# Optimization experiments

Measured on AMD Instinct MI355X. Metric: run time of the kernel, lower is better.

The kernel has to match this reference:

```python
import jax, jax.numpy as jnp
import numpy as np

B, V, J, H, W = 32, 2, 17, 128, 128
TEMP = 0.05   # SoftArgmax2D softmax_temp
EPS = 1e-12


def _soft_argmax(hm):
    # hm: (B*V, J, H, W) -> homogeneous coords (B*V, 3, J), per-joint max value
    bv, j, h, w = hm.shape
    p = jax.nn.softmax(hm.reshape(bv, j, h * w) / TEMP, axis=-1).reshape(bv, j, h, w)
    xs = jnp.arange(w, dtype=hm.dtype)
    ys = jnp.arange(h, dtype=hm.dtype)
    x = jnp.einsum('bjhw,w->bj', p, xs)
    y = jnp.einsum('bjhw,h->bj', p, ys)
    coords = jnp.stack([x, y, jnp.ones_like(x)], axis=1)  # (bv, 3, j)
    maxv = hm.max(axis=(-2, -1))
    return coords, maxv


def _skew(t):
    # t: (..., 3) -> skew-symmetric (..., 3, 3), matches -t_mat^T + t_mat in source
    tx, ty, tz = t[..., 0], t[..., 1], t[..., 2]
    z = jnp.zeros_like(tx)
    return jnp.stack([jnp.stack([z, -tz, ty], -1),
                      jnp.stack([tz, z, -tx], -1),
                      jnp.stack([-ty, tx, z], -1)], -2)


def _forward(origin_hms, AP_K, AP_T, LAT_K, LAT_T):
    K = jnp.stack([AP_K, LAT_K], axis=1)              # (B,V,3,3)
    T = jnp.stack([AP_T, LAT_T], axis=1)              # (B,V,4,4)
    R = T[:, :, :3, :3]
    t_std = T[:, :, :3, 3]                            # (B,V,3) standard_cam_T

    # fundamental matrices for all ordered pairs: cam1 = view j, cam2 = view i
    r = jnp.einsum('bimk,bjnk->bijmn', R, R)          # R_i @ R_j^T
    t = t_std[:, :, None, :] - jnp.einsum('bijmn,bjn->bijm', r, t_std)
    M = jnp.einsum('bijmn,bijnk->bijmk', _skew(t), r)
    invK = jnp.linalg.inv(K)
    # F = invK_i^T @ [t]x @ r @ invK_j
    F = jnp.einsum('bipm,bijpq,bjql->bijml', invK, M, invK)  # (B,V,V,3,3)

    coords, maxv = _soft_argmax(origin_hms)           # (B*V,3,J), (B*V,J)
    inv_aff = jnp.diag(jnp.asarray([4.0, 4.0, 1.0], dtype=origin_hms.dtype))  # inverse of 0.25 scale
    img = jnp.einsum('mn,bvnj->bvmj', inv_aff, coords.reshape(B, V, 3, J))
    confi = maxv.reshape(B, V, J)

    # epipolar distances, fully vectorized over (b, i, j) pairs
    l = jnp.einsum('bijmn,bjnk->bijmk', F, img)       # epipolar lines in view i from joints of view j
    cv = img[:, :, None]                              # (B,V,1,3,J)
    num = jnp.sum(cv * l, axis=3) ** 2                # (B,V,V,J)
    lp = jnp.einsum('bijnm,bink->bijmk', F, img)      # F^T @ cv_joints
    div = l[..., 0, :] ** 2 + l[..., 1, :] ** 2 + lp[..., 0, :] ** 2 + lp[..., 1, :] ** 2
    dist_full = jnp.sqrt(num / (div + EPS))           # (B,V,V,J)

    others = np.asarray([[j for j in range(V) if j != i] for i in range(V)])  # (V,V-1)
    ii = np.repeat(np.arange(V)[:, None], V - 1, axis=1)
    distances = dist_full[:, ii, others]              # (B,V,V-1,J)

    # stand-in for ViewWeightNet: confidence minus mean epipolar error, softmax over views
    score = confi - distances.mean(axis=2)            # (B,V,J)
    vw = jax.nn.softmax(score, axis=1)                # (B,V,J)

    mv = jnp.where(maxv > 0.01, maxv, 1e6).reshape(B * V, J, 1, 1)
    hms_norm = origin_hms / mv
    hm4 = hms_norm.reshape(B, V, J, H, W)

    # cat order: self heatmap first, then other views (matches get_warp_weight / cat_hm layout)
    order = np.asarray([[i] + [j for j in range(V) if j != i] for i in range(V)])  # (V,V)
    cat_hm = hm4[:, order]                            # (B,V,V,J,H,W); identity-warp stand-in for CamFusionModule
    ww = vw[:, order]                                 # (B,V,V,J) warp weights
    fused_hm = jnp.sum(ww[..., None, None] * cat_hm, axis=2).reshape(B * V, J, H, W)

    coords2, _ = _soft_argmax(fused_hm)
    img2 = jnp.einsum('mn,bvnj->bvmj', inv_aff, coords2.reshape(B, V, 3, J))
    return img2[:, :, :2, :], fused_hm


def setup_inputs() -> dict:
    key = jax.random.key(0)
    k1, k2, k3, k4, k5 = jax.random.split(key, 5)
    hms = jax.random.uniform(k1, (B * V, J, H, W), dtype=jnp.float32)

    def make_K(k):
        f = 1000.0 + jax.random.normal(k, (B,)) * 10.0
        Km = jnp.zeros((B, 3, 3), dtype=jnp.float32)
        Km = Km.at[:, 0, 0].set(f).at[:, 1, 1].set(f)
        Km = Km.at[:, 0, 2].set(256.0).at[:, 1, 2].set(256.0).at[:, 2, 2].set(1.0)
        return Km

    def make_T(k):
        A = jax.random.normal(k, (B, 3, 3))
        Q, _ = jnp.linalg.qr(A)
        Q = Q * jnp.linalg.det(Q)[:, None, None]  # force det = +1 (proper rotation)
        t = jax.random.normal(jax.random.fold_in(k, 1), (B, 3, 1)) * 0.1 + jnp.asarray([0.0, 0.0, 5.0]).reshape(3, 1)
        bottom = jnp.tile(jnp.asarray([[[0.0, 0.0, 0.0, 1.0]]]), (B, 1, 1))
        return jnp.concatenate([jnp.concatenate([Q, t], axis=2), bottom], axis=1).astype(jnp.float32)

    return {"origin_hms": hms, "AP_K": make_K(k2), "AP_T": make_T(k3),
            "LAT_K": make_K(k4), "LAT_T": make_T(k5)}


def reference(origin_hms, AP_K, AP_T, LAT_K, LAT_T):
    return _forward(origin_hms, AP_K, AP_T, LAT_K, LAT_T)
```

## Files before the change

kernel.cpp:

```cpp
#include <hip/hip_runtime.h>
#include <math.h>

#define NB 32
#define NV 2
#define NJ 17
#define NH 128
#define NW 128
#define MAPN (NH * NW)
#define MAPN4 (MAPN / 4)
#define NMAPS (NB * NV * NJ)
#define NBJ (NB * NJ)
#define OUT0N (NB * NV * 2 * NJ)
#define INV_TEMP 20.0f
#define EPS_D 1e-12f

typedef float vfloat4 __attribute__((ext_vector_type(4)));

__device__ __forceinline__ float waveMax(float v) {
#pragma unroll
    for (int off = 32; off > 0; off >>= 1)
        v = fmaxf(v, __shfl_xor(v, off, 64));
    return v;
}
__device__ __forceinline__ float waveSum(float v) {
#pragma unroll
    for (int off = 32; off > 0; off >>= 1)
        v += __shfl_xor(v, off, 64);
    return v;
}

__device__ __forceinline__ void inv3(const float K[3][3], float o[3][3]) {
    const float a = K[0][0], b = K[0][1], c = K[0][2];
    const float d = K[1][0], e = K[1][1], f = K[1][2];
    const float g = K[2][0], h = K[2][1], i = K[2][2];
    const float A =  (e * i - f * h);
    const float Bv = -(d * i - f * g);
    const float C =  (d * h - e * g);
    const float det = a * A + b * Bv + c * C;
    const float id = 1.0f / det;
    o[0][0] = A * id;  o[0][1] = -(b * i - c * h) * id;  o[0][2] = (b * f - c * e) * id;
    o[1][0] = Bv * id; o[1][1] = (a * i - c * g) * id;   o[1][2] = -(a * f - c * d) * id;
    o[2][0] = C * id;  o[2][1] = -(a * h - b * g) * id;  o[2][2] = (a * e - b * d) * id;
}

__global__ __launch_bounds__(512, 2) void k_one(const float* __restrict__ hms,
                                                const float* __restrict__ APK,
                                                const float* __restrict__ APT,
                                                const float* __restrict__ LATK,
                                                const float* __restrict__ LATT,
                                                float* __restrict__ out) {
    const int blk = blockIdx.x;
    const int b = blk / NJ, j = blk % NJ;
    const int tid = threadIdx.x;
    const int wid = tid >> 6, lane = tid & 63;

    float F[2][3][3];
    {
        float Km[2][3][3], R[2][3][3], tr[2][3], iK[2][3][3];
        for (int r = 0; r < 3; ++r)
            for (int c = 0; c < 3; ++c) {
                Km[0][r][c] = APK[b * 9 + r * 3 + c];
                Km[1][r][c] = LATK[b * 9 + r * 3 + c];
                R[0][r][c] = APT[b * 16 + r * 4 + c];
                R[1][r][c] = LATT[b * 16 + r * 4 + c];
            }
        for (int r = 0; r < 3; ++r) {
            tr[0][r] = APT[b * 16 + r * 4 + 3];
            tr[1][r] = LATT[b * 16 + r * 4 + 3];
        }
        inv3(Km[0], iK[0]);
        inv3(Km[1], iK[1]);

        for (int i = 0; i < 2; ++i) {
            const int jj = 1 - i;
            float r[3][3];
            for (int m = 0; m < 3; ++m)
                for (int n = 0; n < 3; ++n)
                    r[m][n] = R[i][m][0] * R[jj][n][0] + R[i][m][1] * R[jj][n][1] + R[i][m][2] * R[jj][n][2];
            float tv[3];
            for (int m = 0; m < 3; ++m)
                tv[m] = tr[i][m] - (r[m][0] * tr[jj][0] + r[m][1] * tr[jj][1] + r[m][2] * tr[jj][2]);
            const float S[3][3] = {{0.f, -tv[2], tv[1]}, {tv[2], 0.f, -tv[0]}, {-tv[1], tv[0], 0.f}};
            float M[3][3];
            for (int m = 0; m < 3; ++m)
                for (int n = 0; n < 3; ++n)
                    M[m][n] = S[m][0] * r[0][n] + S[m][1] * r[1][n] + S[m][2] * r[2][n];
            float tmp[3][3];
            for (int p = 0; p < 3; ++p)
                for (int l = 0; l < 3; ++l)
                    tmp[p][l] = M[p][0] * iK[jj][0][l] + M[p][1] * iK[jj][1][l] + M[p][2] * iK[jj][2][l];
            for (int m = 0; m < 3; ++m)
                for (int l = 0; l < 3; ++l)
                    F[i][m][l] = iK[i][0][m] * tmp[0][l] + iK[i][1][m] * tmp[1][l] + iK[i][2][m] * tmp[2][l];
        }
    }

    const int idx0 = (b * 2 + 0) * NJ + j;
    const int idx1 = (b * 2 + 1) * NJ + j;
    const size_t m0 = (size_t)idx0 * MAPN4;
    const size_t m1 = (size_t)idx1 * MAPN4;
    const float4* A  = (const float4*)hms + m0;
    const float4* Bp = (const float4*)hms + m1;

    float4 va[8];
    float mx0 = -1e30f, s0 = 0.f, sx0 = 0.f, sy0 = 0.f;
    float mx1 = -1e30f, s1 = 0.f, sx1 = 0.f, sy1 = 0.f;
#pragma unroll
    for (int u = 0; u < 8; ++u) {
        const int i4 = tid + u * 512;
        const float4 v = A[i4];
        const float4 w = Bp[i4];
        va[u] = v;
        const int e0 = i4 * 4;
        const float hh = (float)(e0 >> 7);
        const float ww = (float)(e0 & 127);
        {
            mx0 = fmaxf(mx0, fmaxf(fmaxf(v.x, v.y), fmaxf(v.z, v.w)));
            const float ea = __expf((v.x - 1.0f) * INV_TEMP);
            const float eb = __expf((v.y - 1.0f) * INV_TEMP);
            const float ec = __expf((v.z - 1.0f) * INV_TEMP);
            const float ed = __expf((v.w - 1.0f) * INV_TEMP);
            const float se = (ea + eb) + (ec + ed);
            s0 += se; sy0 += se * hh;
            sx0 += ea * ww + eb * (ww + 1.f) + ec * (ww + 2.f) + ed * (ww + 3.f);
        }
        {
            mx1 = fmaxf(mx1, fmaxf(fmaxf(w.x, w.y), fmaxf(w.z, w.w)));
            const float ea = __expf((w.x - 1.0f) * INV_TEMP);
            const float eb = __expf((w.y - 1.0f) * INV_TEMP);
            const float ec = __expf((w.z - 1.0f) * INV_TEMP);
            const float ed = __expf((w.w - 1.0f) * INV_TEMP);
            const float se = (ea + eb) + (ec + ed);
            s1 += se; sy1 += se * hh;
            sx1 += ea * ww + eb * (ww + 1.f) + ec * (ww + 2.f) + ed * (ww + 3.f);
        }
    }

    __shared__ float red[8][8];
    mx0 = waveMax(mx0); mx1 = waveMax(mx1);
    s0 = waveSum(s0); sx0 = waveSum(sx0); sy0 = waveSum(sy0);
    s1 = waveSum(s1); sx1 = waveSum(sx1); sy1 = waveSum(sy1);
    if (lane == 0) {
        red[0][wid] = mx0; red[1][wid] = s0; red[2][wid] = sx0; red[3][wid] = sy0;
        red[4][wid] = mx1; red[5][wid] = s1; red[6][wid] = sx1; red[7][wid] = sy1;
    }
    __syncthreads();
    float M0 = red[0][0], S0 = red[1][0], SX0 = red[2][0], SY0 = red[3][0];
    float M1 = red[4][0], S1 = red[5][0], SX1 = red[6][0], SY1 = red[7][0];
#pragma unroll
    for (int w = 1; w < 8; ++w) {
        M0 = fmaxf(M0, red[0][w]); S0 += red[1][w]; SX0 += red[2][w]; SY0 += red[3][w];
        M1 = fmaxf(M1, red[4][w]); S1 += red[5][w]; SX1 += red[6][w]; SY1 += red[7][w];
    }

    float w0, w1;
    {
        const float conf[2] = {M0, M1};
        float img[2][3];
        img[0][0] = 4.0f * (SX0 / S0); img[0][1] = 4.0f * (SY0 / S0); img[0][2] = 1.0f;
        img[1][0] = 4.0f * (SX1 / S1); img[1][1] = 4.0f * (SY1 / S1); img[1][2] = 1.0f;

        float score[2];
        for (int i = 0; i < 2; ++i) {
            const int jj = 1 - i;
            const float l0 = F[i][0][0] * img[jj][0] + F[i][0][1] * img[jj][1] + F[i][0][2] * img[jj][2];
            const float l1 = F[i][1][0] * img[jj][0] + F[i][1][1] * img[jj][1] + F[i][1][2] * img[jj][2];
            const float l2 = F[i][2][0] * img[jj][0] + F[i][2][1] * img[jj][1] + F[i][2][2] * img[jj][2];
            const float sdot = img[i][0] * l0 + img[i][1] * l1 + img[i][2] * l2;
            const float num = sdot * sdot;
            const float lp0 = F[i][0][0] * img[i][0] + F[i][1][0] * img[i][1] + F[i][2][0] * img[i][2];
            const float lp1 = F[i][0][1] * img[i][0] + F[i][1][1] * img[i][1] + F[i][2][1] * img[i][2];
            const float dv = l0 * l0 + l1 * l1 + lp0 * lp0 + lp1 * lp1;
            score[i] = conf[i] - sqrtf(num / (dv + EPS_D));
        }
        const float mS = fmaxf(score[0], score[1]);
        const float e0w = __expf(score[0] - mS), e1w = __expf(score[1] - mS);
        const float inv = 1.0f / (e0w + e1w);
        const float mv0 = conf[0] > 0.01f ? conf[0] : 1e6f;
        const float mv1 = conf[1] > 0.01f ? conf[1] : 1e6f;
        w0 = (e0w * inv) / mv0;
        w1 = (e1w * inv) / mv1;
    }

    float* outhm = out + OUT0N;
    vfloat4* O0 = reinterpret_cast<vfloat4*>(outhm) + m0;
    vfloat4* O1 = reinterpret_cast<vfloat4*>(outhm) + m1;

    float s = 0.f, sx = 0.f, sy = 0.f;
#pragma unroll
    for (int u = 0; u < 8; ++u) {
        const int i4 = tid + u * 512;
        const float4 a = va[u];
        const float4 c = Bp[i4];
        vfloat4 f;
        f.x = w0 * a.x + w1 * c.x;
        f.y = w0 * a.y + w1 * c.y;
        f.z = w0 * a.z + w1 * c.z;
        f.w = w0 * a.w + w1 * c.w;
        __builtin_nontemporal_store(f, &O0[i4]);
        __builtin_nontemporal_store(f, &O1[i4]);
        const int e0 = i4 * 4;
        const float hh = (float)(e0 >> 7);
        const float ww = (float)(e0 & 127);
        const float ea = __expf((f.x - 1.0f) * INV_TEMP);
        const float eb = __expf((f.y - 1.0f) * INV_TEMP);
        const float ec = __expf((f.z - 1.0f) * INV_TEMP);
        const float ed = __expf((f.w - 1.0f) * INV_TEMP);
        const float se = (ea + eb) + (ec + ed);
        s += se; sy += se * hh;
        sx += ea * ww + eb * (ww + 1.f) + ec * (ww + 2.f) + ed * (ww + 3.f);
    }

    __syncthreads();
    s = waveSum(s); sx = waveSum(sx); sy = waveSum(sy);
    if (lane == 0) { red[0][wid] = s; red[1][wid] = sx; red[2][wid] = sy; }
    __syncthreads();
    if (tid == 0) {
        float S = red[0][0], SX = red[1][0], SY = red[2][0];
#pragma unroll
        for (int w = 1; w < 8; ++w) { S += red[0][w]; SX += red[1][w]; SY += red[2][w]; }
        const float x4 = 4.0f * (SX / S);
        const float y4 = 4.0f * (SY / S);
        out[((b * 2 + 0) * 2 + 0) * NJ + j] = x4;
        out[((b * 2 + 0) * 2 + 1) * NJ + j] = y4;
        out[((b * 2 + 1) * 2 + 0) * NJ + j] = x4;
        out[((b * 2 + 1) * 2 + 1) * NJ + j] = y4;
    }
}

extern "C" void kernel_launch(void* const* d_in, const int* in_sizes, int n_in,
                              void* d_out, int out_size, void* d_ws, size_t ws_size,
                              hipStream_t stream) {
    const float* hms  = (const float*)d_in[0];
    const float* APK  = (const float*)d_in[1];
    const float* APT  = (const float*)d_in[2];
    const float* LATK = (const float*)d_in[3];
    const float* LATT = (const float*)d_in[4];
    float* out = (float*)d_out;

    k_one<<<NBJ, 512, 0, stream>>>(hms, APK, APT, LATK, LATT, out);
}
```

Before: 136.6 us.

## Split fused kernel into four chunked kernels for more parallelism via workspace

```diff
diff --git a/kernel.cpp b/kernel.cpp
--- a/kernel.cpp
+++ b/kernel.cpp
@@ -14,6 +14,16 @@
 #define INV_TEMP 20.0f
 #define EPS_D 1e-12f
 
+#define S_CHUNKS 4
+#define S_F4 (MAPN4 / S_CHUNKS)
+#define F_CHUNKS 8
+#define F_F4 (MAPN4 / F_CHUNKS)
+
+#define WS_STATS_B (NMAPS * S_CHUNKS * 16)
+#define WS_W_B (NBJ * 2 * 4)
+#define WS_F_B (NBJ * F_CHUNKS * 16)
+#define WS_NEEDED (WS_STATS_B + WS_W_B + WS_F_B)
+
 typedef float vfloat4 __attribute__((ext_vector_type(4)));
 
 __device__ __forceinline__ float waveMax(float v) {
@@ -41,6 +51,210 @@
     o[0][0] = A * id;  o[0][1] = -(b * i - c * h) * id;  o[0][2] = (b * f - c * e) * id;
     o[1][0] = Bv * id; o[1][1] = (a * i - c * g) * id;   o[1][2] = -(a * f - c * d) * id;
     o[2][0] = C * id;  o[2][1] = -(a * h - b * g) * id;  o[2][2] = (a * e - b * d) * id;
+}
+
+__global__ __launch_bounds__(256, 4) void k_stats(const float* __restrict__ hms,
+                                                  float* __restrict__ ws) {
+    const int blk = blockIdx.x;
+    const int mi = blk >> 2, c = blk & 3;
+    const int tid = threadIdx.x, wid = tid >> 6, lane = tid & 63;
+    const float4* A = (const float4*)hms + (size_t)mi * MAPN4 + (size_t)c * S_F4;
+
+    float mx = -1e30f, s = 0.f, sx = 0.f, sy = 0.f;
+#pragma unroll
+    for (int k = 0; k < 4; ++k) {
+        const int i4 = tid + k * 256;
+        const float4 v = A[i4];
+        const int e0 = (c * S_F4 + i4) * 4;
+        const float hh = (float)(e0 >> 7);
+        const float ww = (float)(e0 & 127);
+        mx = fmaxf(mx, fmaxf(fmaxf(v.x, v.y), fmaxf(v.z, v.w)));
+        const float ea = __expf((v.x - 1.0f) * INV_TEMP);
+        const float eb = __expf((v.y - 1.0f) * INV_TEMP);
+        const float ec = __expf((v.z - 1.0f) * INV_TEMP);
+        const float ed = __expf((v.w - 1.0f) * INV_TEMP);
+        const float se = (ea + eb) + (ec + ed);
+        s += se; sy += se * hh;
+        sx += ea * ww + eb * (ww + 1.f) + ec * (ww + 2.f) + ed * (ww + 3.f);
+    }
+
+    mx = waveMax(mx); s = waveSum(s); sx = waveSum(sx); sy = waveSum(sy);
+    __shared__ float red[4][4];
+    if (lane == 0) { red[0][wid] = mx; red[1][wid] = s; red[2][wid] = sx; red[3][wid] = sy; }
+    __syncthreads();
+    if (tid == 0) {
+        float M = red[0][0], S = red[1][0], SX = red[2][0], SY = red[3][0];
+#pragma unroll
+        for (int w = 1; w < 4; ++w) {
+            M = fmaxf(M, red[0][w]); S += red[1][w]; SX += red[2][w]; SY += red[3][w];
+        }
+        ((float4*)ws)[blk] = make_float4(M, S, SX, SY);
+    }
+}
+
+__global__ void k_weights(const float* __restrict__ ws_stats,
+                          const float* __restrict__ APK, const float* __restrict__ APT,
+                          const float* __restrict__ LATK, const float* __restrict__ LATT,
+                          float* __restrict__ wsw) {
+    const int bj = blockIdx.x * 64 + threadIdx.x;
+    if (bj >= NBJ) return;
+    const int b = bj / NJ, j = bj % NJ;
+
+    float conf[2], img[2][3];
+    const float4* st = (const float4*)ws_stats;
+#pragma unroll
+    for (int v = 0; v < 2; ++v) {
+        const int mi = (b * 2 + v) * NJ + j;
+        float M = -1e30f, S = 0.f, SX = 0.f, SY = 0.f;
+#pragma unroll
+        for (int c = 0; c < S_CHUNKS; ++c) {
+            const float4 p = st[mi * S_CHUNKS + c];
+            M = fmaxf(M, p.x); S += p.y; SX += p.z; SY += p.w;
+        }
+        conf[v] = M;
+        img[v][0] = 4.0f * (SX / S);
+        img[v][1] = 4.0f * (SY / S);
+        img[v][2] = 1.0f;
+    }
+
+    float F[2][3][3];
+    {
+        float Km[2][3][3], R[2][3][3], tr[2][3], iK[2][3][3];
+        for (int r = 0; r < 3; ++r)
+            for (int cc = 0; cc < 3; ++cc) {
+                Km[0][r][cc] = APK[b * 9 + r * 3 + cc];
+                Km[1][r][cc] = LATK[b * 9 + r * 3 + cc];
+                R[0][r][cc] = APT[b * 16 + r * 4 + cc];
+                R[1][r][cc] = LATT[b * 16 + r * 4 + cc];
+            }
+        for (int r = 0; r < 3; ++r) {
+            tr[0][r] = APT[b * 16 + r * 4 + 3];
+            tr[1][r] = LATT[b * 16 + r * 4 + 3];
+        }
+        inv3(Km[0], iK[0]);
+        inv3(Km[1], iK[1]);
+
+        for (int i = 0; i < 2; ++i) {
+            const int jj = 1 - i;
+            float r[3][3];
+            for (int m = 0; m < 3; ++m)
+                for (int n = 0; n < 3; ++n)
+                    r[m][n] = R[i][m][0] * R[jj][n][0] + R[i][m][1] * R[jj][n][1] + R[i][m][2] * R[jj][n][2];
+            float tv[3];
+            for (int m = 0; m < 3; ++m)
+                tv[m] = tr[i][m] - (r[m][0] * tr[jj][0] + r[m][1] * tr[jj][1] + r[m][2] * tr[jj][2]);
+            const float S[3][3] = {{0.f, -tv[2], tv[1]}, {tv[2], 0.f, -tv[0]}, {-tv[1], tv[0], 0.f}};
+            float M[3][3];
+            for (int m = 0; m < 3; ++m)
+                for (int n = 0; n < 3; ++n)
+                    M[m][n] = S[m][0] * r[0][n] + S[m][1] * r[1][n] + S[m][2] * r[2][n];
+            float tmp[3][3];
+            for (int p = 0; p < 3; ++p)
+                for (int l = 0; l < 3; ++l)
+                    tmp[p][l] = M[p][0] * iK[jj][0][l] + M[p][1] * iK[jj][1][l] + M[p][2] * iK[jj][2][l];
+            for (int m = 0; m < 3; ++m)
+                for (int l = 0; l < 3; ++l)
+                    F[i][m][l] = iK[i][0][m] * tmp[0][l] + iK[i][1][m] * tmp[1][l] + iK[i][2][m] * tmp[2][l];
+        }
+    }
+
+    float score[2];
+#pragma unroll
+    for (int i = 0; i < 2; ++i) {
+        const int jj = 1 - i;
+        const float l0 = F[i][0][0] * img[jj][0] + F[i][0][1] * img[jj][1] + F[i][0][2] * img[jj][2];
+        const float l1 = F[i][1][0] * img[jj][0] + F[i][1][1] * img[jj][1] + F[i][1][2] * img[jj][2];
+        const float l2 = F[i][2][0] * img[jj][0] + F[i][2][1] * img[jj][1] + F[i][2][2] * img[jj][2];
+        const float sdot = img[i][0] * l0 + img[i][1] * l1 + img[i][2] * l2;
+        const float num = sdot * sdot;
+        const float lp0 = F[i][0][0] * img[i][0] + F[i][1][0] * img[i][1] + F[i][2][0] * img[i][2];
+        const float lp1 = F[i][0][1] * img[i][0] + F[i][1][1] * img[i][1] + F[i][2][1] * img[i][2];
+        const float dv = l0 * l0 + l1 * l1 + lp0 * lp0 + lp1 * lp1;
+        score[i] = conf[i] - sqrtf(num / (dv + EPS_D));
+    }
+    const float mS = fmaxf(score[0], score[1]);
+    const float e0w = __expf(score[0] - mS), e1w = __expf(score[1] - mS);
+    const float inv = 1.0f / (e0w + e1w);
+    const float mv0 = conf[0] > 0.01f ? conf[0] : 1e6f;
+    const float mv1 = conf[1] > 0.01f ? conf[1] : 1e6f;
+    wsw[bj * 2 + 0] = (e0w * inv) / mv0;
+    wsw[bj * 2 + 1] = (e1w * inv) / mv1;
+}
+
+__global__ __launch_bounds__(256, 4) void k_fuse(const float* __restrict__ hms,
+                                                 const float* __restrict__ wsw,
+                                                 float* __restrict__ out,
+                                                 float* __restrict__ wsf) {
+    const int blk = blockIdx.x;
+    const int bj = blk >> 3, c = blk & 7;
+    const int b = bj / NJ, j = bj % NJ;
+    const int tid = threadIdx.x, wid = tid >> 6, lane = tid & 63;
+
+    const float w0 = wsw[bj * 2 + 0];
+    const float w1 = wsw[bj * 2 + 1];
+
+    const size_t m0 = ((size_t)(b * 2 + 0) * NJ + j) * MAPN4;
+    const size_t m1 = ((size_t)(b * 2 + 1) * NJ + j) * MAPN4;
+    const float4* A  = (const float4*)hms + m0 + (size_t)c * F_F4;
+    const float4* Bp = (const float4*)hms + m1 + (size_t)c * F_F4;
+    float* outhm = out + OUT0N;
+    vfloat4* O0 = reinterpret_cast<vfloat4*>(outhm) + m0 + (size_t)c * F_F4;
+    vfloat4* O1 = reinterpret_cast<vfloat4*>(outhm) + m1 + (size_t)c * F_F4;
+
+    float s = 0.f, sx = 0.f, sy = 0.f;
+#pragma unroll
+    for (int k = 0; k < 2; ++k) {
+        const int i4 = tid + k * 256;
+        const float4 a = A[i4];
+        const float4 cc = Bp[i4];
+        vfloat4 f;
+        f.x = w0 * a.x + w1 * cc.x;
+        f.y = w0 * a.y + w1 * cc.y;
+        f.z = w0 * a.z + w1 * cc.z;
+        f.w = w0 * a.w + w1 * cc.w;
+        __builtin_nontemporal_store(f, &O0[i4]);
+        __builtin_nontemporal_store(f, &O1[i4]);
+        const int e0 = (c * F_F4 + i4) * 4;
+        const float hh = (float)(e0 >> 7);
+        const float ww = (float)(e0 & 127);
+        const float ea = __expf((f.x - 1.0f) * INV_TEMP);
+        const float eb = __expf((f.y - 1.0f) * INV_TEMP);
+        const float ec = __expf((f.z - 1.0f) * INV_TEMP);
+        const float ed = __expf((f.w - 1.0f) * INV_TEMP);
+        const float se = (ea + eb) + (ec + ed);
+        s += se; sy += se * hh;
+        sx += ea * ww + eb * (ww + 1.f) + ec * (ww + 2.f) + ed * (ww + 3.f);
+    }
+
+    s = waveSum(s); sx = waveSum(sx); sy = waveSum(sy);
+    __shared__ float red[3][4];
+    if (lane == 0) { red[0][wid] = s; red[1][wid] = sx; red[2][wid] = sy; }
+    __syncthreads();
+    if (tid == 0) {
+        float S = red[0][0], SX = red[1][0], SY = red[2][0];
+#pragma unroll
+        for (int w = 1; w < 4; ++w) { S += red[0][w]; SX += red[1][w]; SY += red[2][w]; }
+        ((float4*)wsf)[blk] = make_float4(S, SX, SY, 0.f);
+    }
+}
+
+__global__ void k_out(const float* __restrict__ wsf, float* __restrict__ out) {
+    const int bj = blockIdx.x * 64 + threadIdx.x;
+    if (bj >= NBJ) return;
+    const int b = bj / NJ, j = bj % NJ;
+    const float4* p = (const float4*)wsf + bj * F_CHUNKS;
+    float S = 0.f, SX = 0.f, SY = 0.f;
+#pragma unroll
+    for (int c = 0; c < F_CHUNKS; ++c) {
+        const float4 q = p[c];
+        S += q.x; SX += q.y; SY += q.z;
+    }
+    const float x4 = 4.0f * (SX / S);
+    const float y4 = 4.0f * (SY / S);
+    out[((b * 2 + 0) * 2 + 0) * NJ + j] = x4;
+    out[((b * 2 + 0) * 2 + 1) * NJ + j] = y4;
+    out[((b * 2 + 1) * 2 + 0) * NJ + j] = x4;
+    out[((b * 2 + 1) * 2 + 1) * NJ + j] = y4;
 }
 
 __global__ __launch_bounds__(512, 2) void k_one(const float* __restrict__ hms,
@@ -238,5 +452,15 @@
     const float* LATT = (const float*)d_in[4];
     float* out = (float*)d_out;
 
-    k_one<<<NBJ, 512, 0, stream>>>(hms, APK, APT, LATK, LATT, out);
-}
+    if (d_ws != nullptr && ws_size >= (size_t)WS_NEEDED) {
+        float* ws_stats = (float*)d_ws;
+        float* ws_w = ws_stats + NMAPS * S_CHUNKS * 4;
+        float* ws_f = ws_w + NBJ * 2;
+        k_stats<<<NMAPS * S_CHUNKS, 256, 0, stream>>>(hms, ws_stats);
+        k_weights<<<(NBJ + 63) / 64, 64, 0, stream>>>(ws_stats, APK, APT, LATK, LATT, ws_w);
+        k_fuse<<<NBJ * F_CHUNKS, 256, 0, stream>>>(hms, ws_w, out, ws_f);
+        k_out<<<(NBJ + 63) / 64, 64, 0, stream>>>(ws_f, out);
+    } else {
+        k_one<<<NBJ, 512, 0, stream>>>(hms, APK, APT, LATK, LATT, out);
+    }
+}
```

New measurement: 141.9 us. 1.04x slower.
